# Performance work log

Measured on AMD Instinct MI355X. Metric: run time of the kernel, lower is better.

Reference implementation:

```python
import jax, jax.numpy as jnp
import numpy as np

N, D, C, E, K = 100000, 64, 40, 1600000, 2

def setup_inputs() -> dict:
    key = jax.random.key(0)
    k1, k2, k3 = jax.random.split(key, 3)
    x = jax.random.normal(k1, (N, D), dtype=jnp.float32)
    edge_index = jax.random.randint(k2, (2, E), 0, N, dtype=jnp.int64)
    W = jax.random.normal(k3, (D, C), dtype=jnp.float32) * 0.05
    b = jnp.zeros((C,), dtype=jnp.float32)
    return {"x": x, "edge_index": edge_index, "W": W, "b": b}

def reference(x, edge_index, W, b):
    n = x.shape[0]
    self_loop = jnp.arange(n, dtype=edge_index.dtype)
    row = jnp.concatenate([edge_index[0], self_loop])  # [E+N]
    col = jnp.concatenate([edge_index[1], self_loop])  # [E+N]
    # degree over row (out-degree incl. self loops), as in torch_geometric.utils.degree
    deg = jax.ops.segment_sum(jnp.ones_like(row, dtype=x.dtype), row, num_segments=n)
    deg_inv_sqrt = jnp.where(deg > 0, jax.lax.rsqrt(deg), 0.0)
    norm = deg_inv_sqrt[row] * deg_inv_sqrt[col]  # [E+N]
    # K hops of SpMM: out[r] += norm_e * x[c] for each edge e=(r,c)
    for _ in range(K):
        x = jax.ops.segment_sum(norm[:, None] * x[col], row, num_segments=n)
    logits = x @ W + b  # [N, C]
    return jax.nn.log_softmax(logits, axis=1)
```

## Files before the change

kernel.cpp:

```cpp
#include <hip/hip_runtime.h>
#include <math.h>


#define D_FEAT 64
#define NCLS 40
#define BROWS 256
#define BROWS_LOG 8
#define BINCAP 4608
#define CSRCAP 5376
#define EPT 25
#define NBLK 256

__device__ __forceinline__ unsigned pack_bf16_2(float lo, float hi) {
    unsigned ulo = __float_as_uint(lo);
    unsigned uhi = __float_as_uint(hi);
    ulo = (ulo + 0x7fffu + ((ulo >> 16) & 1u)) >> 16;
    uhi = (uhi + 0x7fffu + ((uhi >> 16) & 1u)) & 0xffff0000u;
    return uhi | ulo;
}

__device__ __forceinline__ void acc2(unsigned u, float& a, float& b) {
    a += __uint_as_float(u << 16);
    b += __uint_as_float(u & 0xffff0000u);
}

__global__ __launch_bounds__(256) void count_edges_kernel(const int* __restrict__ rows,
                                                          int* __restrict__ blockcounts,
                                                          int e, int nb) {
    __shared__ int cnt[512];
    for (int i = threadIdx.x; i < nb; i += 256) cnt[i] = 0;
    __syncthreads();
    int base = blockIdx.x * (256 * EPT) + threadIdx.x;
#pragma unroll
    for (int k = 0; k < EPT; k++) {
        int idx = base + k * 256;
        if (idx < e) atomicAdd(&cnt[rows[idx] >> BROWS_LOG], 1);
    }
    __syncthreads();
    for (int i = threadIdx.x; i < nb; i += 256)
        blockcounts[i * NBLK + blockIdx.x] = cnt[i];
}

__global__ __launch_bounds__(256) void scan_bases_kernel(int* __restrict__ blockcounts,
                                                         int* __restrict__ bucket_total,
                                                         int nblocks) {
    __shared__ int sm[256];
    int b = blockIdx.x;
    int t = threadIdx.x;
    int v = (t < nblocks) ? blockcounts[b * NBLK + t] : 0;
    sm[t] = v;
    __syncthreads();
    for (int off = 1; off < 256; off <<= 1) {
        int x = (t >= off) ? sm[t - off] : 0;
        __syncthreads();
        sm[t] += x;
        __syncthreads();
    }
    if (t < nblocks) blockcounts[b * NBLK + t] = sm[t] - v;
    if (t == 255) bucket_total[b] = sm[255];
}

__global__ __launch_bounds__(256) void scatter_edges_kernel(const int* __restrict__ rows,
                                                            const int* __restrict__ cols,
                                                            const int* __restrict__ blockcounts,
                                                            unsigned* __restrict__ bins,
                                                            int e, int nb) {
    __shared__ int cur[512];
    for (int i = threadIdx.x; i < nb; i += 256)
        cur[i] = blockcounts[i * NBLK + blockIdx.x];
    __syncthreads();
    int base = blockIdx.x * (256 * EPT) + threadIdx.x;
#pragma unroll
    for (int k = 0; k < EPT; k++) {
        int idx = base + k * 256;
        if (idx < e) {
            int r = rows[idx];
            int b = r >> BROWS_LOG;
            int pos = atomicAdd(&cur[b], 1);
            bins[(size_t)b * BINCAP + pos] =
                ((unsigned)(r & (BROWS - 1)) << 17) | (unsigned)cols[idx];
        }
    }
}

__global__ __launch_bounds__(256) void build_csr_kernel(const unsigned* __restrict__ bins,
                                                        const int* __restrict__ bucket_total,
                                                        int* __restrict__ csr_col,
                                                        uint2* __restrict__ row_info,
                                                        float* __restrict__ dis, int n) {
    __shared__ int cnt[BROWS];
    __shared__ int sm[BROWS];
    __shared__ int cur[BROWS];
    __shared__ int lcsr[CSRCAP];
    int b = blockIdx.x;
    int tid = threadIdx.x;
    int m = bucket_total[b];
    cnt[tid] = 0;
    __syncthreads();
    const unsigned* bp = bins + (size_t)b * BINCAP;
    for (int i = tid; i < m; i += 256) atomicAdd(&cnt[bp[i] >> 17], 1);
    __syncthreads();
    int c = cnt[tid];
    int padded = (c + 3) & ~3;
    int r = b * BROWS + tid;
    if (r < n) dis[r] = rsqrtf(1.0f + (float)c);
    sm[tid] = padded;
    __syncthreads();
    for (int off = 1; off < 256; off <<= 1) {
        int t = (tid >= off) ? sm[tid - off] : 0;
        __syncthreads();
        sm[tid] += t;
        __syncthreads();
    }
    int off0 = sm[tid] - padded;
    cur[tid] = off0;
    if (r < n) row_info[r] = make_uint2((unsigned)(b * CSRCAP + off0), (unsigned)padded);
    __syncthreads();
    for (int i = tid; i < m; i += 256) {
        unsigned u = bp[i];
        int pos = atomicAdd(&cur[u >> 17], 1);
        lcsr[pos] = (int)(u & 0x1FFFFu);
    }
    __syncthreads();
    for (int i2 = off0 + 1; i2 < off0 + c; i2++) {
        int key = lcsr[i2];
        int j = i2 - 1;
        while (j >= off0 && lcsr[j] > key) { lcsr[j + 1] = lcsr[j]; j--; }
        lcsr[j + 1] = key;
    }
    for (int j = off0 + c; j < off0 + padded; j++) lcsr[j] = n;
    __syncthreads();
    int tot = sm[BROWS - 1];
    int4* cp4 = (int4*)(csr_col + (size_t)b * CSRCAP);
    const int4* l4 = (const int4*)lcsr;
    for (int i = tid; i < (tot >> 2); i += 256) cp4[i] = l4[i];
}

__global__ void scale_x_kernel(const float* __restrict__ x, const float* __restrict__ dis,
                               unsigned* __restrict__ xs0, unsigned* __restrict__ xs1, int n) {
    int i = blockIdx.x * blockDim.x + threadIdx.x;
    int total = (n + 1) * (D_FEAT / 2);
    if (i >= total) return;
    int node = i >> 5;
    if (node < n) {
        float s = dis[node];
        float2 v = ((const float2*)x)[i];
        xs0[i] = pack_bf16_2(s * v.x, s * v.y);
    } else {
        xs0[i] = 0u;
        xs1[i] = 0u;
    }
}

#define GATHER16(cp, xs_in, ql, base, len)                                  \
    uint2 u0 = make_uint2(0u, 0u), u1 = u0, u2 = u0, u3 = u0;               \
    uint2 u4 = u0, u5 = u0, u6 = u0, u7 = u0;                               \
    uint2 u8 = u0, u9 = u0, u10 = u0, u11 = u0;                             \
    uint2 u12 = u0, u13 = u0, u14 = u0, u15 = u0;                           \
    if (base < len) {                                                       \
        uint4 cv = cp[(base >> 2) + 0];                                     \
        u0 = xs_in[cv.x * 16 + ql]; u1 = xs_in[cv.y * 16 + ql];             \
        u2 = xs_in[cv.z * 16 + ql]; u3 = xs_in[cv.w * 16 + ql];             \
    }                                                                       \
    if (base + 4 < len) {                                                   \
        uint4 cv = cp[(base >> 2) + 1];                                     \
        u4 = xs_in[cv.x * 16 + ql]; u5 = xs_in[cv.y * 16 + ql];             \
        u6 = xs_in[cv.z * 16 + ql]; u7 = xs_in[cv.w * 16 + ql];             \
    }                                                                       \
    if (base + 8 < len) {                                                   \
        uint4 cv = cp[(base >> 2) + 2];                                     \
        u8 = xs_in[cv.x * 16 + ql]; u9 = xs_in[cv.y * 16 + ql];             \
        u10 = xs_in[cv.z * 16 + ql]; u11 = xs_in[cv.w * 16 + ql];           \
    }                                                                       \
    if (base + 12 < len) {                                                  \
        uint4 cv = cp[(base >> 2) + 3];                                     \
        u12 = xs_in[cv.x * 16 + ql]; u13 = xs_in[cv.y * 16 + ql];           \
        u14 = xs_in[cv.z * 16 + ql]; u15 = xs_in[cv.w * 16 + ql];           \
    }                                                                       \
    acc2(u0.x, h0, h1); acc2(u0.y, h2, h3);                                 \
    acc2(u1.x, h0, h1); acc2(u1.y, h2, h3);                                 \
    acc2(u2.x, h0, h1); acc2(u2.y, h2, h3);                                 \
    acc2(u3.x, h0, h1); acc2(u3.y, h2, h3);                                 \
    acc2(u4.x, h0, h1); acc2(u4.y, h2, h3);                                 \
    acc2(u5.x, h0, h1); acc2(u5.y, h2, h3);                                 \
    acc2(u6.x, h0, h1); acc2(u6.y, h2, h3);                                 \
    acc2(u7.x, h0, h1); acc2(u7.y, h2, h3);                                 \
    acc2(u8.x, h0, h1); acc2(u8.y, h2, h3);                                 \
    acc2(u9.x, h0, h1); acc2(u9.y, h2, h3);                                 \
    acc2(u10.x, h0, h1); acc2(u10.y, h2, h3);                               \
    acc2(u11.x, h0, h1); acc2(u11.y, h2, h3);                               \
    acc2(u12.x, h0, h1); acc2(u12.y, h2, h3);                               \
    acc2(u13.x, h0, h1); acc2(u13.y, h2, h3);                               \
    acc2(u14.x, h0, h1); acc2(u14.y, h2, h3);                               \
    acc2(u15.x, h0, h1); acc2(u15.y, h2, h3);

__global__ __launch_bounds__(256) void spmm_hop1_kernel(const uint2* __restrict__ xs_in,
                                                        uint2* __restrict__ xs_out,
                                                        const uint2* __restrict__ row_info,
                                                        const int* __restrict__ csr_col,
                                                        const float* __restrict__ dis, int n) {
    int wave = (blockIdx.x * blockDim.x + threadIdx.x) >> 6;
    int lane = threadIdx.x & 63;
    int q = lane >> 4, ql = lane & 15;
    int r = wave * 4 + q;
    bool valid = r < n;
    int s = 0, len = 0;
    if (valid) { uint2 info = row_info[r]; s = (int)info.x; len = (int)info.y; }
    int maxlen = len;
    maxlen = max(maxlen, __shfl_xor(maxlen, 16, 64));
    maxlen = max(maxlen, __shfl_xor(maxlen, 32, 64));

    float h0 = 0.f, h1 = 0.f, h2 = 0.f, h3 = 0.f;
    const uint4* cp = (const uint4*)(csr_col + s);
    for (int base = 0; base < maxlen; base += 16) {
        GATHER16(cp, xs_in, ql, base, len)
    }
    if (valid) {
        uint2 us = xs_in[r * 16 + ql];
        acc2(us.x, h0, h1); acc2(us.y, h2, h3);
        float dr = dis[r];
        float dr2 = dr * dr;
        xs_out[r * 16 + ql] = make_uint2(pack_bf16_2(dr2 * h0, dr2 * h1),
                                         pack_bf16_2(dr2 * h2, dr2 * h3));
    }
}

__global__ __launch_bounds__(256) void spmm_logits_kernel(const uint2* __restrict__ xs_in,
                                                          const uint2* __restrict__ row_info,
                                                          const int* __restrict__ csr_col,
                                                          const float* __restrict__ dis,
                                                          const float* __restrict__ W,
                                                          const float* __restrict__ b,
                                                          float* __restrict__ out, int n) {
    __shared__ float Wl[D_FEAT * NCLS];
    __shared__ float bl[NCLS];
    for (int i = threadIdx.x; i < D_FEAT * NCLS; i += blockDim.x) Wl[i] = W[i];
    for (int i = threadIdx.x; i < NCLS; i += blockDim.x) bl[i] = b[i];
    __syncthreads();

    int wave = (blockIdx.x * blockDim.x + threadIdx.x) >> 6;
    int lane = threadIdx.x & 63;
    int q = lane >> 4, ql = lane & 15;
    int r = wave * 4 + q;
    bool valid = r < n;
    int s = 0, len = 0;
    if (valid) { uint2 info = row_info[r]; s = (int)info.x; len = (int)info.y; }
    int maxlen = len;
    maxlen = max(maxlen, __shfl_xor(maxlen, 16, 64));
    maxlen = max(maxlen, __shfl_xor(maxlen, 32, 64));

    float h0 = 0.f, h1 = 0.f, h2 = 0.f, h3 = 0.f;
    const uint4* cp = (const uint4*)(csr_col + s);
    for (int base = 0; base < maxlen; base += 16) {
        GATHER16(cp, xs_in, ql, base, len)
    }

    float y0, y1, y2;
    {
        uint2 us = valid ? xs_in[r * 16 + ql] : make_uint2(0u, 0u);
        acc2(us.x, h0, h1); acc2(us.y, h2, h3);
        float dr = valid ? dis[r] : 0.f;
        h0 *= dr; h1 *= dr; h2 *= dr; h3 *= dr;

        int c0 = ql, c1 = ql + 16;
        int c2 = (ql < 8) ? (ql + 32) : ql;
        y0 = bl[c0]; y1 = bl[c1]; y2 = bl[c2];
        int qbase = q << 4;
#pragma unroll
        for (int d = 0; d < D_FEAT; d++) {
            int src = qbase + (d >> 2);
            float xv;
            switch (d & 3) {
                case 0: xv = __shfl(h0, src, 64); break;
                case 1: xv = __shfl(h1, src, 64); break;
                case 2: xv = __shfl(h2, src, 64); break;
                default: xv = __shfl(h3, src, 64); break;
            }
            y0 += xv * Wl[d * NCLS + c0];
            y1 += xv * Wl[d * NCLS + c1];
            y2 += xv * Wl[d * NCLS + c2];
        }
    }

    bool has3 = (ql < 8);
    float m = fmaxf(y0, y1);
    if (has3) m = fmaxf(m, y2);
#pragma unroll
    for (int o = 8; o > 0; o >>= 1) m = fmaxf(m, __shfl_xor(m, o, 64));
    float sm = __expf(y0 - m) + __expf(y1 - m) + (has3 ? __expf(y2 - m) : 0.f);
#pragma unroll
    for (int o = 8; o > 0; o >>= 1) sm += __shfl_xor(sm, o, 64);
    float lse = m + __logf(sm);

    if (valid) {
        float* op = out + (long long)r * NCLS;
        op[ql] = y0 - lse;
        op[ql + 16] = y1 - lse;
        if (has3) op[ql + 32] = y2 - lse;
    }
}

extern "C" void kernel_launch(void* const* d_in, const int* in_sizes, int n_in,
                              void* d_out, int out_size, void* d_ws, size_t ws_size,
                              hipStream_t stream) {
    const float* x  = (const float*)d_in[0];
    const int*   ei = (const int*)d_in[1];
    const float* W  = (const float*)d_in[2];
    const float* b  = (const float*)d_in[3];
    float* out = (float*)d_out;

    const int n = in_sizes[0] / D_FEAT;
    const int e = in_sizes[1] / 2;
    const int nb = (n + BROWS - 1) / BROWS;
    const int eblocks = (e + 256 * EPT - 1) / (256 * EPT);

    const int* rows = ei;
    const int* cols = ei + e;

    size_t na = ((size_t)n + 256) & ~(size_t)255;
    int*      bucket_total = (int*)d_ws;
    int*      blockcounts  = bucket_total + 512;
    float*    dis          = (float*)(blockcounts + (size_t)nb * NBLK + 256);
    uint2*    row_info     = (uint2*)(dis + na);
    unsigned* bins         = (unsigned*)(row_info + na);
    int*      csr_col      = (int*)(bins + (size_t)nb * BINCAP);
    unsigned* xs0          = (unsigned*)(csr_col + (size_t)nb * CSRCAP + 256);
    unsigned* xs1          = xs0 + (size_t)(n + 1) * (D_FEAT / 2);

    const int BS = 256;

    count_edges_kernel<<<eblocks, BS, 0, stream>>>(rows, blockcounts, e, nb);
    scan_bases_kernel<<<nb, BS, 0, stream>>>(blockcounts, bucket_total, eblocks);
    scatter_edges_kernel<<<eblocks, BS, 0, stream>>>(rows, cols, blockcounts, bins, e, nb);
    build_csr_kernel<<<nb, BS, 0, stream>>>(bins, bucket_total, csr_col, row_info, dis, n);
    {
        int tot = (n + 1) * (D_FEAT / 2);
        scale_x_kernel<<<(tot + BS - 1) / BS, BS, 0, stream>>>(x, dis, xs0, xs1, n);
    }

    int nwaves = (n + 3) / 4;
    int blocks = (nwaves * 64 + BS - 1) / BS;
    spmm_hop1_kernel<<<blocks, BS, 0, stream>>>((const uint2*)xs0, (uint2*)xs1,
                                                row_info, csr_col, dis, n);
    spmm_logits_kernel<<<blocks, BS, 0, stream>>>((const uint2*)xs1, row_info, csr_col,
                                                  dis, W, b, out, n);
}
```

Baseline: 255.3 us.

## Apply W projection before propagation and parallelize per-row CSR sort with bitonic

Moves the linear layer ahead of the two SpMM hops, so each gather propagates 40-class bf16 vectors instead of 64-feature vectors. This cuts gather bytes per edge and removes the in-loop GEMV and W staging from the logits kernel. The CSR build replaces a per-thread insertion sort with a per-row wavefront bitonic sort, falling back to a serial sort for long rows. It also changes rounding order, since bf16 now stores the projected values, and splits storage into 32- and 8-column arrays, which adds a second gather per edge.

```diff
diff --git a/kernel.cpp b/kernel.cpp
--- a/kernel.cpp
+++ b/kernel.cpp
@@ -122,181 +122,195 @@
         lcsr[pos] = (int)(u & 0x1FFFFu);
     }
     __syncthreads();
-    for (int i2 = off0 + 1; i2 < off0 + c; i2++) {
-        int key = lcsr[i2];
-        int j = i2 - 1;
-        while (j >= off0 && lcsr[j] > key) { lcsr[j + 1] = lcsr[j]; j--; }
-        lcsr[j + 1] = key;
-    }
-    for (int j = off0 + c; j < off0 + padded; j++) lcsr[j] = n;
-    __syncthreads();
-    int tot = sm[BROWS - 1];
-    int4* cp4 = (int4*)(csr_col + (size_t)b * CSRCAP);
-    const int4* l4 = (const int4*)lcsr;
-    for (int i = tid; i < (tot >> 2); i += 256) cp4[i] = l4[i];
-}
-
-__global__ void scale_x_kernel(const float* __restrict__ x, const float* __restrict__ dis,
-                               unsigned* __restrict__ xs0, unsigned* __restrict__ xs1, int n) {
-    int i = blockIdx.x * blockDim.x + threadIdx.x;
-    int total = (n + 1) * (D_FEAT / 2);
-    if (i >= total) return;
-    int node = i >> 5;
-    if (node < n) {
-        float s = dis[node];
-        float2 v = ((const float2*)x)[i];
-        xs0[i] = pack_bf16_2(s * v.x, s * v.y);
-    } else {
-        xs0[i] = 0u;
-        xs1[i] = 0u;
-    }
-}
-
-#define GATHER16(cp, xs_in, ql, base, len)                                  \
-    uint2 u0 = make_uint2(0u, 0u), u1 = u0, u2 = u0, u3 = u0;               \
-    uint2 u4 = u0, u5 = u0, u6 = u0, u7 = u0;                               \
-    uint2 u8 = u0, u9 = u0, u10 = u0, u11 = u0;                             \
-    uint2 u12 = u0, u13 = u0, u14 = u0, u15 = u0;                           \
-    if (base < len) {                                                       \
-        uint4 cv = cp[(base >> 2) + 0];                                     \
-        u0 = xs_in[cv.x * 16 + ql]; u1 = xs_in[cv.y * 16 + ql];             \
-        u2 = xs_in[cv.z * 16 + ql]; u3 = xs_in[cv.w * 16 + ql];             \
-    }                                                                       \
-    if (base + 4 < len) {                                                   \
-        uint4 cv = cp[(base >> 2) + 1];                                     \
-        u4 = xs_in[cv.x * 16 + ql]; u5 = xs_in[cv.y * 16 + ql];             \
-        u6 = xs_in[cv.z * 16 + ql]; u7 = xs_in[cv.w * 16 + ql];             \
-    }                                                                       \
-    if (base + 8 < len) {                                                   \
-        uint4 cv = cp[(base >> 2) + 2];                                     \
-        u8 = xs_in[cv.x * 16 + ql]; u9 = xs_in[cv.y * 16 + ql];             \
-        u10 = xs_in[cv.z * 16 + ql]; u11 = xs_in[cv.w * 16 + ql];           \
-    }                                                                       \
-    if (base + 12 < len) {                                                  \
-        uint4 cv = cp[(base >> 2) + 3];                                     \
-        u12 = xs_in[cv.x * 16 + ql]; u13 = xs_in[cv.y * 16 + ql];           \
-        u14 = xs_in[cv.z * 16 + ql]; u15 = xs_in[cv.w * 16 + ql];           \
-    }                                                                       \
-    acc2(u0.x, h0, h1); acc2(u0.y, h2, h3);                                 \
-    acc2(u1.x, h0, h1); acc2(u1.y, h2, h3);                                 \
-    acc2(u2.x, h0, h1); acc2(u2.y, h2, h3);                                 \
-    acc2(u3.x, h0, h1); acc2(u3.y, h2, h3);                                 \
-    acc2(u4.x, h0, h1); acc2(u4.y, h2, h3);                                 \
-    acc2(u5.x, h0, h1); acc2(u5.y, h2, h3);                                 \
-    acc2(u6.x, h0, h1); acc2(u6.y, h2, h3);                                 \
-    acc2(u7.x, h0, h1); acc2(u7.y, h2, h3);                                 \
-    acc2(u8.x, h0, h1); acc2(u8.y, h2, h3);                                 \
-    acc2(u9.x, h0, h1); acc2(u9.y, h2, h3);                                 \
-    acc2(u10.x, h0, h1); acc2(u10.y, h2, h3);                               \
-    acc2(u11.x, h0, h1); acc2(u11.y, h2, h3);                               \
-    acc2(u12.x, h0, h1); acc2(u12.y, h2, h3);                               \
-    acc2(u13.x, h0, h1); acc2(u13.y, h2, h3);                               \
-    acc2(u14.x, h0, h1); acc2(u14.y, h2, h3);                               \
-    acc2(u15.x, h0, h1); acc2(u15.y, h2, h3);
-
-__global__ __launch_bounds__(256) void spmm_hop1_kernel(const uint2* __restrict__ xs_in,
-                                                        uint2* __restrict__ xs_out,
+    int wv = tid >> 6, lane = tid & 63;
+    int* gcsr = csr_col + (size_t)b * CSRCAP;
+    for (int rowi = wv; rowi < BROWS; rowi += 4) {
+        int cc = cnt[rowi];
+        int pp = (cc + 3) & ~3;
+        if (pp == 0) continue;
+        int o0 = sm[rowi] - pp;
+        if (pp <= 64) {
+            int v = (lane < cc) ? lcsr[o0 + lane] : n;
+#pragma unroll
+            for (int k = 2; k <= 64; k <<= 1) {
+#pragma unroll
+                for (int j = k >> 1; j > 0; j >>= 1) {
+                    int other = __shfl_xor(v, j, 64);
+                    bool up = ((lane & k) == 0);
+                    bool takeMin = (((lane & j) == 0) == up);
+                    v = takeMin ? min(v, other) : max(v, other);
+                }
+            }
+            if (lane < pp) gcsr[o0 + lane] = v;
+        } else {
+            if (lane == 0) {
+                for (int i2 = o0 + 1; i2 < o0 + cc; i2++) {
+                    int key = lcsr[i2];
+                    int j = i2 - 1;
+                    while (j >= o0 && lcsr[j] > key) { lcsr[j + 1] = lcsr[j]; j--; }
+                    lcsr[j + 1] = key;
+                }
+                for (int j = o0 + cc; j < o0 + pp; j++) lcsr[j] = n;
+            }
+            for (int i2 = lane; i2 < pp; i2 += 64) gcsr[o0 + i2] = lcsr[o0 + i2];
+        }
+    }
+}
+
+__global__ __launch_bounds__(256) void gemv_y_kernel(const float* __restrict__ x,
+                                                     const float* __restrict__ W,
+                                                     const float* __restrict__ dis,
+                                                     unsigned* __restrict__ ya,
+                                                     unsigned* __restrict__ yb, int n) {
+    __shared__ float Wl[D_FEAT * NCLS];
+    for (int i = threadIdx.x; i < D_FEAT * NCLS; i += 256) Wl[i] = W[i];
+    __syncthreads();
+    int wave = (blockIdx.x * blockDim.x + threadIdx.x) >> 6;
+    int lane = threadIdx.x & 63;
+    int q = lane >> 4, ql = lane & 15;
+    int r = wave * 4 + q;
+    if (r > n) return;
+    if (r == n) {
+        ya[(size_t)n * 16 + ql] = 0u;
+        if (ql < 4) yb[(size_t)n * 4 + ql] = 0u;
+        return;
+    }
+    float4 xv = ((const float4*)(x + (size_t)r * D_FEAT))[ql];
+    int c0 = 2 * ql, c1 = 2 * ql + 1;
+    bool hb = ql < 4;
+    int c2 = hb ? (32 + 2 * ql) : 0;
+    int c3 = hb ? (33 + 2 * ql) : 1;
+    float y0 = 0.f, y1 = 0.f, y2 = 0.f, y3 = 0.f;
+    int qbase = q << 4;
+#pragma unroll
+    for (int d = 0; d < D_FEAT; d++) {
+        int src = qbase + (d >> 2);
+        float xd;
+        switch (d & 3) {
+            case 0: xd = __shfl(xv.x, src, 64); break;
+            case 1: xd = __shfl(xv.y, src, 64); break;
+            case 2: xd = __shfl(xv.z, src, 64); break;
+            default: xd = __shfl(xv.w, src, 64); break;
+        }
+        y0 += xd * Wl[d * NCLS + c0];
+        y1 += xd * Wl[d * NCLS + c1];
+        y2 += xd * Wl[d * NCLS + c2];
+        y3 += xd * Wl[d * NCLS + c3];
+    }
+    float dr = dis[r];
+    ya[(size_t)r * 16 + ql] = pack_bf16_2(dr * y0, dr * y1);
+    if (hb) yb[(size_t)r * 4 + ql] = pack_bf16_2(dr * y2, dr * y3);
+}
+
+__device__ __forceinline__ void gather16(const uint4* __restrict__ cp,
+                                         const unsigned* __restrict__ Ya,
+                                         const unsigned* __restrict__ Yb,
+                                         int ql, int qlb, int base, int len,
+                                         float& a0, float& a1, float& b0, float& b1) {
+    unsigned ua[16], ub[16];
+#pragma unroll
+    for (int i = 0; i < 16; i++) { ua[i] = 0u; ub[i] = 0u; }
+#pragma unroll
+    for (int g = 0; g < 4; g++) {
+        if (base + 4 * g < len) {
+            uint4 cv = cp[(base >> 2) + g];
+            ua[4 * g + 0] = Ya[cv.x * 16 + ql]; ub[4 * g + 0] = Yb[cv.x * 4 + qlb];
+            ua[4 * g + 1] = Ya[cv.y * 16 + ql]; ub[4 * g + 1] = Yb[cv.y * 4 + qlb];
+            ua[4 * g + 2] = Ya[cv.z * 16 + ql]; ub[4 * g + 2] = Yb[cv.z * 4 + qlb];
+            ua[4 * g + 3] = Ya[cv.w * 16 + ql]; ub[4 * g + 3] = Yb[cv.w * 4 + qlb];
+        }
+    }
+#pragma unroll
+    for (int i = 0; i < 16; i++) { acc2(ua[i], a0, a1); acc2(ub[i], b0, b1); }
+}
+
+__global__ __launch_bounds__(256) void spmm_hop1_kernel(const unsigned* __restrict__ ya_in,
+                                                        const unsigned* __restrict__ yb_in,
+                                                        unsigned* __restrict__ ya_out,
+                                                        unsigned* __restrict__ yb_out,
                                                         const uint2* __restrict__ row_info,
                                                         const int* __restrict__ csr_col,
                                                         const float* __restrict__ dis, int n) {
     int wave = (blockIdx.x * blockDim.x + threadIdx.x) >> 6;
     int lane = threadIdx.x & 63;
-    int q = lane >> 4, ql = lane & 15;
+    int q = lane >> 4, ql = lane & 15, qlb = ql & 3;
     int r = wave * 4 + q;
     bool valid = r < n;
     int s = 0, len = 0;
-    if (valid) { uint2 info = row_info[r]; s = (int)info.x; len = (int)info.y; }
+    if (valid) { uint2 iv = row_info[r]; s = (int)iv.x; len = (int)iv.y; }
     int maxlen = len;
     maxlen = max(maxlen, __shfl_xor(maxlen, 16, 64));
     maxlen = max(maxlen, __shfl_xor(maxlen, 32, 64));
 
-    float h0 = 0.f, h1 = 0.f, h2 = 0.f, h3 = 0.f;
+    float a0 = 0.f, a1 = 0.f, b0 = 0.f, b1 = 0.f;
     const uint4* cp = (const uint4*)(csr_col + s);
-    for (int base = 0; base < maxlen; base += 16) {
-        GATHER16(cp, xs_in, ql, base, len)
-    }
+    for (int base = 0; base < maxlen; base += 16)
+        gather16(cp, ya_in, yb_in, ql, qlb, base, len, a0, a1, b0, b1);
+
     if (valid) {
-        uint2 us = xs_in[r * 16 + ql];
-        acc2(us.x, h0, h1); acc2(us.y, h2, h3);
+        acc2(ya_in[(size_t)r * 16 + ql], a0, a1);
+        acc2(yb_in[(size_t)r * 4 + qlb], b0, b1);
         float dr = dis[r];
         float dr2 = dr * dr;
-        xs_out[r * 16 + ql] = make_uint2(pack_bf16_2(dr2 * h0, dr2 * h1),
-                                         pack_bf16_2(dr2 * h2, dr2 * h3));
-    }
-}
-
-__global__ __launch_bounds__(256) void spmm_logits_kernel(const uint2* __restrict__ xs_in,
+        ya_out[(size_t)r * 16 + ql] = pack_bf16_2(dr2 * a0, dr2 * a1);
+        if (ql < 4) yb_out[(size_t)r * 4 + ql] = pack_bf16_2(dr2 * b0, dr2 * b1);
+    } else if (r == n) {
+        ya_out[(size_t)n * 16 + ql] = 0u;
+        if (ql < 4) yb_out[(size_t)n * 4 + ql] = 0u;
+    }
+}
+
+__global__ __launch_bounds__(256) void spmm_logits_kernel(const unsigned* __restrict__ ya_in,
+                                                          const unsigned* __restrict__ yb_in,
                                                           const uint2* __restrict__ row_info,
                                                           const int* __restrict__ csr_col,
                                                           const float* __restrict__ dis,
-                                                          const float* __restrict__ W,
-                                                          const float* __restrict__ b,
+                                                          const float* __restrict__ bias,
                                                           float* __restrict__ out, int n) {
-    __shared__ float Wl[D_FEAT * NCLS];
-    __shared__ float bl[NCLS];
-    for (int i = threadIdx.x; i < D_FEAT * NCLS; i += blockDim.x) Wl[i] = W[i];
-    for (int i = threadIdx.x; i < NCLS; i += blockDim.x) bl[i] = b[i];
-    __syncthreads();
-
     int wave = (blockIdx.x * blockDim.x + threadIdx.x) >> 6;
     int lane = threadIdx.x & 63;
-    int q = lane >> 4, ql = lane & 15;
+    int q = lane >> 4, ql = lane & 15, qlb = ql & 3;
+    bool hb = ql < 4;
+    float bv0 = bias[2 * ql], bv1 = bias[2 * ql + 1];
+    float bv2 = hb ? bias[32 + 2 * ql] : 0.f;
+    float bv3 = hb ? bias[33 + 2 * ql] : 0.f;
+
     int r = wave * 4 + q;
     bool valid = r < n;
     int s = 0, len = 0;
-    if (valid) { uint2 info = row_info[r]; s = (int)info.x; len = (int)info.y; }
+    if (valid) { uint2 iv = row_info[r]; s = (int)iv.x; len = (int)iv.y; }
     int maxlen = len;
     maxlen = max(maxlen, __shfl_xor(maxlen, 16, 64));
     maxlen = max(maxlen, __shfl_xor(maxlen, 32, 64));
 
-    float h0 = 0.f, h1 = 0.f, h2 = 0.f, h3 = 0.f;
+    float a0 = 0.f, a1 = 0.f, b0 = 0.f, b1 = 0.f;
     const uint4* cp = (const uint4*)(csr_col + s);
-    for (int base = 0; base < maxlen; base += 16) {
-        GATHER16(cp, xs_in, ql, base, len)
-    }
-
-    float y0, y1, y2;
-    {
-        uint2 us = valid ? xs_in[r * 16 + ql] : make_uint2(0u, 0u);
-        acc2(us.x, h0, h1); acc2(us.y, h2, h3);
-        float dr = valid ? dis[r] : 0.f;
-        h0 *= dr; h1 *= dr; h2 *= dr; h3 *= dr;
-
-        int c0 = ql, c1 = ql + 16;
-        int c2 = (ql < 8) ? (ql + 32) : ql;
-        y0 = bl[c0]; y1 = bl[c1]; y2 = bl[c2];
-        int qbase = q << 4;
-#pragma unroll
-        for (int d = 0; d < D_FEAT; d++) {
-            int src = qbase + (d >> 2);
-            float xv;
-            switch (d & 3) {
-                case 0: xv = __shfl(h0, src, 64); break;
-                case 1: xv = __shfl(h1, src, 64); break;
-                case 2: xv = __shfl(h2, src, 64); break;
-                default: xv = __shfl(h3, src, 64); break;
-            }
-            y0 += xv * Wl[d * NCLS + c0];
-            y1 += xv * Wl[d * NCLS + c1];
-            y2 += xv * Wl[d * NCLS + c2];
-        }
-    }
-
-    bool has3 = (ql < 8);
-    float m = fmaxf(y0, y1);
-    if (has3) m = fmaxf(m, y2);
+    for (int base = 0; base < maxlen; base += 16)
+        gather16(cp, ya_in, yb_in, ql, qlb, base, len, a0, a1, b0, b1);
+
+    if (valid) {
+        acc2(ya_in[(size_t)r * 16 + ql], a0, a1);
+        acc2(yb_in[(size_t)r * 4 + qlb], b0, b1);
+    }
+    float dr = valid ? dis[r] : 0.f;
+    float l0 = dr * a0 + bv0;
+    float l1 = dr * a1 + bv1;
+    float l2 = hb ? (dr * b0 + bv2) : -INFINITY;
+    float l3 = hb ? (dr * b1 + bv3) : -INFINITY;
+
+    float m = fmaxf(fmaxf(l0, l1), fmaxf(l2, l3));
 #pragma unroll
     for (int o = 8; o > 0; o >>= 1) m = fmaxf(m, __shfl_xor(m, o, 64));
-    float sm = __expf(y0 - m) + __expf(y1 - m) + (has3 ? __expf(y2 - m) : 0.f);
-#pragma unroll
-    for (int o = 8; o > 0; o >>= 1) sm += __shfl_xor(sm, o, 64);
-    float lse = m + __logf(sm);
+    float sme = __expf(l0 - m) + __expf(l1 - m);
+    if (hb) sme += __expf(l2 - m) + __expf(l3 - m);
+#pragma unroll
+    for (int o = 8; o > 0; o >>= 1) sme += __shfl_xor(sme, o, 64);
+    float lse = m + __logf(sme);
 
     if (valid) {
-        float* op = out + (long long)r * NCLS;
-        op[ql] = y0 - lse;
-        op[ql + 16] = y1 - lse;
-        if (has3) op[ql + 32] = y2 - lse;
+        float2* op = (float2*)(out + (size_t)r * NCLS);
+        op[ql] = make_float2(l0 - lse, l1 - lse);
+        if (hb) op[16 + ql] = make_float2(l2 - lse, l3 - lse);
     }
 }
 
@@ -317,15 +331,19 @@
     const int* rows = ei;
     const int* cols = ei + e;
 
-    size_t na = ((size_t)n + 256) & ~(size_t)255;
+    size_t na  = ((size_t)n + 256) & ~(size_t)255;
+    size_t szA = (((size_t)(n + 1) * 16) + 255) & ~(size_t)255;
+    size_t szB = (((size_t)(n + 1) * 4) + 255) & ~(size_t)255;
     int*      bucket_total = (int*)d_ws;
     int*      blockcounts  = bucket_total + 512;
     float*    dis          = (float*)(blockcounts + (size_t)nb * NBLK + 256);
     uint2*    row_info     = (uint2*)(dis + na);
     unsigned* bins         = (unsigned*)(row_info + na);
     int*      csr_col      = (int*)(bins + (size_t)nb * BINCAP);
-    unsigned* xs0          = (unsigned*)(csr_col + (size_t)nb * CSRCAP + 256);
-    unsigned* xs1          = xs0 + (size_t)(n + 1) * (D_FEAT / 2);
+    unsigned* ys0a         = (unsigned*)(csr_col + (size_t)nb * CSRCAP + 256);
+    unsigned* ys0b         = ys0a + szA;
+    unsigned* ys1a         = ys0b + szB;
+    unsigned* ys1b         = ys1a + szA;
 
     const int BS = 256;
 
@@ -333,15 +351,14 @@
     scan_bases_kernel<<<nb, BS, 0, stream>>>(blockcounts, bucket_total, eblocks);
     scatter_edges_kernel<<<eblocks, BS, 0, stream>>>(rows, cols, blockcounts, bins, e, nb);
     build_csr_kernel<<<nb, BS, 0, stream>>>(bins, bucket_total, csr_col, row_info, dis, n);
-    {
-        int tot = (n + 1) * (D_FEAT / 2);
-        scale_x_kernel<<<(tot + BS - 1) / BS, BS, 0, stream>>>(x, dis, xs0, xs1, n);
-    }
-
-    int nwaves = (n + 3) / 4;
-    int blocks = (nwaves * 64 + BS - 1) / BS;
-    spmm_hop1_kernel<<<blocks, BS, 0, stream>>>((const uint2*)xs0, (uint2*)xs1,
-                                                row_info, csr_col, dis, n);
-    spmm_logits_kernel<<<blocks, BS, 0, stream>>>((const uint2*)xs1, row_info, csr_col,
-                                                  dis, W, b, out, n);
-}
+
+    int waves1 = (n + 1 + 3) / 4;
+    int blocks1 = (waves1 * 64 + BS - 1) / BS;
+    gemv_y_kernel<<<blocks1, BS, 0, stream>>>(x, W, dis, ys0a, ys0b, n);
+    spmm_hop1_kernel<<<blocks1, BS, 0, stream>>>(ys0a, ys0b, ys1a, ys1b,
+                                                 row_info, csr_col, dis, n);
+    int waves2 = (n + 3) / 4;
+    int blocks2 = (waves2 * 64 + BS - 1) / BS;
+    spmm_logits_kernel<<<blocks2, BS, 0, stream>>>(ys1a, ys1b, row_info, csr_col,
+                                                   dis, b, out, n);
+}
```

After: 311.8 us. +22.1%, slower.
